# Performance work log

Hardware: AMD Instinct MI355X
Metric: run time of the kernel (lower is better)

Reference implementation:

```python
import jax, jax.numpy as jnp
import numpy as np

B, L, D = 16, 4096, 512
WORD_SIZE = 2048  # codebook_size // 4
WORD_LEN = 2


def setup_inputs() -> dict:
    key = jax.random.key(0)
    k1, k2, k3, k4, k5 = jax.random.split(key, 5)
    char_tokens = jax.random.randint(k1, (B, L), 0, 8192, dtype=jnp.int64 if jax.config.jax_enable_x64 else jnp.int32)
    char_embeddings = jax.random.normal(k2, (B, L, D), dtype=jnp.float32)
    # word_codebook initialized uniform(-1/word_size, 1/word_size) in the original
    word_codebook = jax.random.uniform(k3, (WORD_SIZE, D), dtype=jnp.float32,
                                       minval=-1.0 / WORD_SIZE, maxval=1.0 / WORD_SIZE)
    proj_w = jax.random.normal(k4, (D, D), dtype=jnp.float32) * (1.0 / np.sqrt(D))
    proj_b = jax.random.normal(k5, (D,), dtype=jnp.float32) * 0.01
    return {"char_tokens": char_tokens, "char_embeddings": char_embeddings,
            "word_codebook": word_codebook, "proj_w": proj_w, "proj_b": proj_b}


def reference(char_tokens, char_embeddings, word_codebook, proj_w, proj_b):
    Bv, Lv, Dv = char_embeddings.shape
    G = Lv // WORD_LEN  # number of 2-char groups per sequence
    # mean-pool each consecutive pair of characters -> [B, G, D]
    means = char_embeddings.reshape(Bv, G, WORD_LEN, Dv).mean(axis=2)
    # squared-euclidean nearest codebook entry (same argmin as cdist)
    # d2[b,g,k] = ||m||^2 - 2 m.W^T + ||W||^2 ; ||m||^2 constant over k -> drop
    dots = jnp.einsum('bgd,kd->bgk', means, word_codebook)            # [B,G,K]
    cb_sq = jnp.sum(word_codebook * word_codebook, axis=-1)           # [K]
    word_indices = jnp.argmin(cb_sq[None, None, :] - 2.0 * dots, axis=-1)  # [B,G]
    word_embeddings = word_codebook[word_indices]                     # [B,G,D]
    # alignment loss: mse(proj(word_emb), stop_grad(word_emb))
    projected = jnp.einsum('bgd,ed->bge', word_embeddings, proj_w) + proj_b
    target = jax.lax.stop_gradient(word_embeddings)
    alignment_loss = jnp.mean((projected - target) ** 2)
    return (word_indices, word_embeddings, alignment_loss)
```

## Files before the change

### kernel.cpp

```cpp
#include <hip/hip_runtime.h>


#define D_DIM    512
#define K_CODES  2048
#define N_ROWS   32768
#define EPS_GAP  1e-5f
#define LOSS_SCALE (1.0f / 16777216.0f)

typedef __attribute__((ext_vector_type(8))) short short8;
typedef __attribute__((ext_vector_type(4))) float f32x4;

__device__ __forceinline__ void split_bf16(float f, unsigned short& h, unsigned short& l) {
    unsigned u = __float_as_uint(f);
    h = (unsigned short)(u >> 16);
    float hr = __uint_as_float(u & 0xFFFF0000u);
    l = (unsigned short)(__float_as_uint(f - hr) >> 16);
}

__device__ __forceinline__ void dma16(const void* g, void* l) {
    __builtin_amdgcn_global_load_lds(
        (const __attribute__((address_space(1))) unsigned int*)g,
        (__attribute__((address_space(3))) unsigned int*)l, 16, 0, 0);
}

__device__ __forceinline__ void merge_cand(float s, int idx, float& v1, int& i1, float& v2, int& i2) {
    if (s < v1 || (s == v1 && idx < i1)) { v2 = v1; i2 = i1; v1 = s; i1 = idx; }
    else if (s < v2 || (s == v2 && idx < i2)) { v2 = s; i2 = idx; }
}

__global__ __launch_bounds__(256, 1)
void cra_pack_a(const float* __restrict__ ce,
                unsigned short* __restrict__ Ap)
{
    const int tid = threadIdx.x;
    const int mb  = blockIdx.x;
    const int rq  = tid >> 5;
    const int dq  = tid & 31;
    const int dbase = dq * 16;
    const int ach = dq >> 1;
    const int k0  = (dq & 1) * 16;

    #pragma unroll 2
    for (int p = 0; p < 16; ++p) {
        const int r  = p * 8 + rq;
        const int gr = mb * 128 + r;
        const float* a0 = ce + (size_t)(2 * gr) * D_DIM + dbase;
        const float* a1 = a0 + D_DIM;
        float4 x0[4], x1[4];
        #pragma unroll
        for (int q = 0; q < 4; ++q) {
            x0[q] = *(const float4*)(a0 + q * 4);
            x1[q] = *(const float4*)(a1 + q * 4);
        }
        short8 h8[2], l8[2];
        #pragma unroll
        for (int q = 0; q < 4; ++q) {
            const float m[4] = {0.5f * (x0[q].x + x1[q].x), 0.5f * (x0[q].y + x1[q].y),
                                0.5f * (x0[q].z + x1[q].z), 0.5f * (x0[q].w + x1[q].w)};
            #pragma unroll
            for (int e = 0; e < 4; ++e) {
                unsigned short hh, ll;
                split_bf16(m[e], hh, ll);
                h8[q >> 1][(q & 1) * 4 + e] = (short)hh;
                l8[q >> 1][(q & 1) * 4 + e] = (short)ll;
            }
        }
        const size_t hb = ((size_t)(mb * 32 + ach) * 128 + r) * 32 + k0;
        const size_t lb = ((size_t)(mb * 32 + 16 + ach) * 128 + r) * 32 + k0;
        *(short8*)(Ap + hb)     = h8[0];
        *(short8*)(Ap + hb + 8) = h8[1];
        *(short8*)(Ap + lb)     = l8[0];
        *(short8*)(Ap + lb + 8) = l8[1];
    }
}

__global__ __launch_bounds__(256, 1)
void cra_pack_b(const float* __restrict__ cb,
                unsigned short* __restrict__ Bp,
                float* __restrict__ cb_sq,
                float* __restrict__ Sk,
                int* __restrict__ counter,
                float* __restrict__ loss_out)
{
    __shared__ float cbs[32 * D_DIM];
    const int tid = threadIdx.x;
    const int c0  = blockIdx.x * 32;

    if (blockIdx.x == 0) {
        #pragma unroll
        for (int j = 0; j < 8; ++j) Sk[tid + j * 256] = 0.0f;
        if (tid == 0) { counter[0] = 0; loss_out[0] = 0.0f; }
    }

    {
        const float4* src = (const float4*)(cb + (size_t)c0 * D_DIM);
        float4* dst = (float4*)cbs;
        #pragma unroll
        for (int k = 0; k < 16; ++k) dst[tid + k * 256] = src[tid + k * 256];
    }
    __syncthreads();

    if (tid < 32) {
        const float* r = cbs + tid * D_DIM;
        float s = 0.f;
        for (int d = 0; d < D_DIM; ++d) s = fmaf(r[d], r[d], s);
        cb_sq[c0 + tid] = s;
    }

    const int row  = tid >> 3;
    const int k    = c0 + row;
    const int colb = k >> 7;
    const int pr   = k & 127;
    const int dspan = (tid & 7) * 64;
    #pragma unroll
    for (int g = 0; g < 8; ++g) {
        const int d   = dspan + g * 8;
        const int bch = d >> 5;
        const int k0  = d & 31;
        short8 h8, l8;
        #pragma unroll
        for (int e = 0; e < 8; ++e) {
            unsigned short hh, ll;
            split_bf16(cbs[row * D_DIM + d + e], hh, ll);
            h8[e] = (short)hh; l8[e] = (short)ll;
        }
        *(short8*)(Bp + ((size_t)(colb * 32 + bch) * 128 + pr) * 32 + k0)      = h8;
        *(short8*)(Bp + ((size_t)(colb * 32 + 16 + bch) * 128 + pr) * 32 + k0) = l8;
    }
}

__global__ __launch_bounds__(256, 1)
void cra_proj(const float* __restrict__ cb,
              const float* __restrict__ W,
              const float* __restrict__ pb,
              float* __restrict__ Sk)
{
    __shared__ float cbs[32 * D_DIM];
    __shared__ float red[4 * 32];
    const int tid = threadIdx.x;
    const int cblock = blockIdx.x >> 2;
    const int eb     = blockIdx.x & 3;
    const int c0 = cblock * 32;

    {
        const float4* src = (const float4*)(cb + (size_t)c0 * D_DIM);
        float4* dst = (float4*)cbs;
        #pragma unroll
        for (int k = 0; k < 16; ++k) dst[tid + k * 256] = src[tid + k * 256];
    }
    __syncthreads();

    const int e  = eb * 128 + (tid >> 1);
    const int dh = (tid & 1) * 256;
    float acc[32];
    #pragma unroll
    for (int c = 0; c < 32; ++c) acc[c] = 0.f;
    const float4* wrow = (const float4*)(W + (size_t)e * D_DIM + dh);
    for (int dq = 0; dq < 64; ++dq) {
        const float4 wv = wrow[dq];
        #pragma unroll
        for (int c = 0; c < 32; ++c) {
            const float4 cv = *(const float4*)&cbs[c * D_DIM + dh + dq * 4];
            acc[c] += cv.x * wv.x + cv.y * wv.y + cv.z * wv.z + cv.w * wv.w;
        }
    }
    const float bias = pb[e];
    const int w = tid >> 6;
    #pragma unroll
    for (int c = 0; c < 32; ++c) {
        const float full = acc[c] + __shfl_xor(acc[c], 1);
        const float diff = full + bias - cbs[c * D_DIM + e];
        float v = (tid & 1) ? 0.f : diff * diff;
        #pragma unroll
        for (int off = 32; off > 0; off >>= 1) v += __shfl_down(v, off, 64);
        if ((tid & 63) == 0) red[w * 32 + c] = v;
    }
    __syncthreads();
    if (tid < 32)
        atomicAdd(&Sk[c0 + tid],
                  red[tid] + red[32 + tid] + red[64 + tid] + red[96 + tid]);
}

__global__ __launch_bounds__(1024, 4)
void cra_gemm(const unsigned short* __restrict__ Ap,
              const unsigned short* __restrict__ Bp,
              const float* __restrict__ cb_sq,
              float4* __restrict__ wsRed)
{
    __shared__ __align__(16) char sMem[65536];

    const int tid  = threadIdx.x;
    const int bid  = blockIdx.x;
    const int wgid = (bid & 7) * 128 + (bid >> 3);
    const int mb   = wgid >> 3;
    const int colb = wgid & 7;
    const int rowBase = mb * 256;
    const int colBase = colb * 256;

    const int lane = tid & 63;
    const int w    = tid >> 6;
    const int wm   = w >> 2;
    const int wn   = w & 3;
    const int cid  = lane & 15;
    const int quad = lane >> 4;

    const int rg  = w >> 2;
    const int off = (w & 3) * 2048;
    const char* AgBase = (const char*)Ap + ((size_t)(2 * mb)   * 32) * 8192 + lane * 16;
    const char* BgBase = (const char*)Bp + ((size_t)(2 * colb) * 32) * 8192 + lane * 16;
    const char* gBase  = (rg < 2) ? (AgBase + (rg & 1) * (32 * 8192) + off)
                                  : (BgBase + (rg & 1) * (32 * 8192) + off);
    const int dstOff = (rg >> 1) * 16384 + (rg & 1) * 8192 + off;

    f32x4 acc[4][4];
    #pragma unroll
    for (int i = 0; i < 4; ++i)
        #pragma unroll
        for (int j = 0; j < 4; ++j) acc[i][j] = (f32x4)(0.f);

    auto stage = [&](int g, int p) {
        const int ach = g & 31;
        const int bch = (g & 15) | ((g & 32) >> 1);
        const int ch  = (rg < 2) ? ach : bch;
        const char* src = gBase + ch * 8192;
        char* dst = (char*)sMem + p * 32768 + dstOff;
        dma16(src,        dst);
        dma16(src + 1024, dst + 1024);
    };

    stage(0, 0);
    stage(1, 1);

    #pragma unroll 1
    for (int g = 0; g < 48; ++g) {
        const int p = g & 1;
        if (g < 47) asm volatile("s_waitcnt vmcnt(2)\n\ts_barrier" ::: "memory");
        else        asm volatile("s_waitcnt vmcnt(0)\n\ts_barrier" ::: "memory");

        const short* sA = (const short*)(sMem + p * 32768);
        const short* sB = (const short*)(sMem + p * 32768 + 16384);

        short8 aF[4], bF[4];
        #pragma unroll
        for (int mi = 0; mi < 4; ++mi)
            aF[mi] = *(const short8*)&sA[(wm * 64 + mi * 16 + cid) * 32 + quad * 8];
        #pragma unroll
        for (int ni = 0; ni < 4; ++ni)
            bF[ni] = *(const short8*)&sB[(wn * 64 + ni * 16 + cid) * 32 + quad * 8];
        __builtin_amdgcn_s_setprio(1);
        #pragma unroll
        for (int mi = 0; mi < 4; ++mi)
            #pragma unroll
            for (int ni = 0; ni < 4; ++ni)
                acc[mi][ni] = __builtin_amdgcn_mfma_f32_16x16x32_bf16(aF[mi], bF[ni], acc[mi][ni], 0, 0, 0);
        __builtin_amdgcn_s_setprio(0);

        asm volatile("s_waitcnt lgkmcnt(0)\n\ts_barrier" ::: "memory");

        if (g + 2 < 48) stage(g + 2, p);
    }

    float cq[4];
    #pragma unroll
    for (int ni = 0; ni < 4; ++ni) cq[ni] = cb_sq[colBase + wn * 64 + ni * 16 + cid];

    float4* sRed = (float4*)sMem;
    #pragma unroll
    for (int mi = 0; mi < 4; ++mi) {
        #pragma unroll
        for (int reg = 0; reg < 4; ++reg) {
            float v1 = 3.4e38f, v2 = 3.4e38f;
            int   i1 = 0x7FFFFFFF, i2 = 0x7FFFFFFF;
            #pragma unroll
            for (int ni = 0; ni < 4; ++ni) {
                const float s = fmaf(-2.0f, acc[mi][ni][reg], cq[ni]);
                merge_cand(s, colBase + wn * 64 + ni * 16 + cid, v1, i1, v2, i2);
            }
            #pragma unroll
            for (int d = 1; d <= 2; d <<= 1) {
                float ov1 = __shfl_xor(v1, d); int oi1 = __shfl_xor(i1, d);
                float ov2 = __shfl_xor(v2, d); int oi2 = __shfl_xor(i2, d);
                merge_cand(ov1, oi1, v1, i1, v2, i2);
                merge_cand(ov2, oi2, v1, i1, v2, i2);
            }
            if ((cid & 3) == 0) {
                const int rl = wm * 64 + mi * 16 + quad * 4 + reg;
                sRed[(rl * 4 + wn) * 4 + (cid >> 2)] =
                    make_float4(v1, __int_as_float(i1), v2, __int_as_float(i2));
            }
        }
    }
    __syncthreads();
    if (tid < 256) {
        float v1 = 3.4e38f, v2 = 3.4e38f;
        int   i1 = 0x7FFFFFFF, i2 = 0x7FFFFFFF;
        #pragma unroll
        for (int e = 0; e < 16; ++e) {
            const float4 t = sRed[tid * 16 + e];
            merge_cand(t.x, __float_as_int(t.y), v1, i1, v2, i2);
            merge_cand(t.z, __float_as_int(t.w), v1, i1, v2, i2);
        }
        wsRed[(size_t)(rowBase + tid) * 8 + colb] =
            make_float4(v1, __int_as_float(i1), v2, __int_as_float(i2));
    }
}

__global__ __launch_bounds__(256, 1)
void cra_merge(const float4* __restrict__ wsRed,
               const float* __restrict__ Sk,
               float* __restrict__ out_idx,
               float* __restrict__ out_loss,
               int* __restrict__ counter,
               int* __restrict__ flagRow,
               int2* __restrict__ flagI)
{
    __shared__ float sl[256];
    const int tid = threadIdx.x;
    const int r = blockIdx.x * 256 + tid;
    float v1 = 3.4e38f, v2 = 3.4e38f;
    int   i1 = 0x7FFFFFFF, i2 = 0x7FFFFFFF;
    #pragma unroll 4
    for (int cbk = 0; cbk < 8; ++cbk) {
        const float4 t = wsRed[(size_t)r * 8 + cbk];
        merge_cand(t.x, __float_as_int(t.y), v1, i1, v2, i2);
        merge_cand(t.z, __float_as_int(t.w), v1, i1, v2, i2);
    }
    out_idx[r] = (float)i1;
    if (v2 - v1 < EPS_GAP) {
        const int slot = atomicAdd(counter, 1);
        flagRow[slot] = r;
        flagI[slot] = make_int2(i1, i2);
    }
    sl[tid] = Sk[i1];
    __syncthreads();
    for (int s = 128; s > 0; s >>= 1) { if (tid < s) sl[tid] += sl[tid + s]; __syncthreads(); }
    if (tid == 0) atomicAdd(out_loss, sl[0] * LOSS_SCALE);
}

__global__ __launch_bounds__(256, 1)
void cra_gather(const float* __restrict__ out_idx,
                const float4* __restrict__ cb4,
                float4* __restrict__ out4)
{
    __shared__ int sidx[128];
    const int tid = threadIdx.x;
    const int rb = blockIdx.x * 128;
    if (tid < 128) sidx[tid] = (int)out_idx[rb + tid];
    __syncthreads();
    for (int j = tid; j < 128 * 128; j += 256) {
        const int row = j >> 7, q = j & 127;
        out4[(size_t)(rb + row) * 128 + q] = cb4[(size_t)sidx[row] * 128 + q];
    }
}

__global__ __launch_bounds__(256, 1)
void cra_recheck(const float* __restrict__ ce,
                 const float* __restrict__ cb,
                 const float* __restrict__ cb_sq,
                 const float* __restrict__ Sk,
                 const int* __restrict__ counter,
                 const int* __restrict__ flagRow,
                 const int2* __restrict__ flagI,
                 float* __restrict__ out_idx,
                 float4* __restrict__ out4,
                 float* __restrict__ out_loss,
                 const float4* __restrict__ cb4)
{
    __shared__ float rp[8];
    __shared__ int swin;
    const int tid = threadIdx.x;
    const int n = counter[0];
    for (int f = blockIdx.x; f < n; f += 64) {
        const int row = flagRow[f];
        const int2 ii = flagI[f];
        const int d0 = tid * 2;
        const float2 x0 = *(const float2*)(ce + (size_t)(2 * row) * D_DIM + d0);
        const float2 x1 = *(const float2*)(ce + (size_t)(2 * row) * D_DIM + D_DIM + d0);
        const float m0 = 0.5f * (x0.x + x1.x), m1 = 0.5f * (x0.y + x1.y);
        const float* c1 = cb + (size_t)ii.x * D_DIM + d0;
        const float* c2 = cb + (size_t)ii.y * D_DIM + d0;
        float p1 = fmaf(m0, c1[0], m1 * c1[1]);
        float p2 = fmaf(m0, c2[0], m1 * c2[1]);
        #pragma unroll
        for (int off = 32; off > 0; off >>= 1) {
            p1 += __shfl_down(p1, off, 64);
            p2 += __shfl_down(p2, off, 64);
        }
        if ((tid & 63) == 0) { rp[(tid >> 6) * 2] = p1; rp[(tid >> 6) * 2 + 1] = p2; }
        __syncthreads();
        if (tid == 0) {
            const float dot1 = rp[0] + rp[2] + rp[4] + rp[6];
            const float dot2 = rp[1] + rp[3] + rp[5] + rp[7];
            const float s1 = cb_sq[ii.x] - 2.f * dot1;
            const float s2 = cb_sq[ii.y] - 2.f * dot2;
            const int win = (s2 < s1 || (s2 == s1 && ii.y < ii.x)) ? ii.y : ii.x;
            swin = win;
            if (win != ii.x) {
                out_idx[row] = (float)win;
                atomicAdd(out_loss, (Sk[win] - Sk[ii.x]) * LOSS_SCALE);
            }
        }
        __syncthreads();
        if (swin != ii.x) {
            for (int q = tid; q < 128; q += 256)
                out4[(size_t)row * 128 + q] = cb4[(size_t)swin * 128 + q];
        }
        __syncthreads();
    }
}

extern "C" void kernel_launch(void* const* d_in, const int* in_sizes, int n_in,
                              void* d_out, int out_size, void* d_ws, size_t ws_size,
                              hipStream_t stream)
{
    const float* ce = (const float*)d_in[1];
    const float* cb = (const float*)d_in[2];
    const float* W  = (const float*)d_in[3];
    const float* pb = (const float*)d_in[4];

    char* ws = (char*)d_ws;
    unsigned short* Bp = (unsigned short*)ws;
    float4* wsRed  = (float4*)(ws + 4194304);
    float* cb_sq   = (float*)(ws + 12582912);
    float* Sk      = (float*)(ws + 12582912 + 8192);
    int*   flagRow = (int*)(ws + 12582912 + 16384);
    int2*  flagI   = (int2*)(ws + 12582912 + 16384 + 131072);
    int*   counter = (int*)(ws + 12582912 + 16384 + 131072 + 262144);

    float* out_idx  = (float*)d_out;
    float* out_emb  = out_idx + N_ROWS;
    float* out_loss = out_emb + (size_t)N_ROWS * D_DIM;
    unsigned short* Ap = (unsigned short*)out_emb;

    cra_pack_a<<<256, 256, 0, stream>>>(ce, Ap);
    cra_pack_b<<<64, 256, 0, stream>>>(cb, Bp, cb_sq, Sk, counter, out_loss);
    cra_proj<<<256, 256, 0, stream>>>(cb, W, pb, Sk);
    cra_gemm<<<1024, 1024, 0, stream>>>(Ap, Bp, cb_sq, wsRed);
    cra_merge<<<128, 256, 0, stream>>>(wsRed, Sk, out_idx, out_loss, counter, flagRow, flagI);
    cra_gather<<<256, 256, 0, stream>>>(out_idx, (const float4*)cb, (float4*)out_emb);
    cra_recheck<<<64, 256, 0, stream>>>(ce, cb, cb_sq, Sk, counter, flagRow, flagI,
                                        out_idx, (float4*)out_emb, out_loss, (const float4*)cb);
}
```

Measured before the change: 938.6 us.

## Shrink GEMM tile to 128x256 with triple-buffered LDS prefetch

Halves the row tile of the distance GEMM to 128 rows using 512-thread blocks and twice as many blocks. The LDS pipeline moves from double to triple buffering, with the next-but-one stage issued right after the barrier instead of at the loop end, so loads overlap more of the MFMA work. Smaller blocks may raise occupancy and help latency hiding, but they reload codebook tiles more often, raising global traffic per output.

```diff
diff --git a/kernel.cpp b/kernel.cpp
--- a/kernel.cpp
+++ b/kernel.cpp
@@ -181,21 +181,21 @@
                   red[tid] + red[32 + tid] + red[64 + tid] + red[96 + tid]);
 }
 
-__global__ __launch_bounds__(1024, 4)
+__global__ __launch_bounds__(512, 4)
 void cra_gemm(const unsigned short* __restrict__ Ap,
               const unsigned short* __restrict__ Bp,
               const float* __restrict__ cb_sq,
               float4* __restrict__ wsRed)
 {
-    __shared__ __align__(16) char sMem[65536];
+    __shared__ __align__(16) char sMem[3 * 24576];
 
     const int tid  = threadIdx.x;
     const int bid  = blockIdx.x;
-    const int wgid = (bid & 7) * 128 + (bid >> 3);
+    const int wgid = (bid & 7) * 256 + (bid >> 3);
     const int mb   = wgid >> 3;
-    const int colb = wgid & 7;
-    const int rowBase = mb * 256;
-    const int colBase = colb * 256;
+    const int cb   = wgid & 7;
+    const int rowBase = mb * 128;
+    const int colBase = cb * 256;
 
     const int lane = tid & 63;
     const int w    = tid >> 6;
@@ -204,28 +204,30 @@
     const int cid  = lane & 15;
     const int quad = lane >> 4;
 
-    const int rg  = w >> 2;
-    const int off = (w & 3) * 2048;
-    const char* AgBase = (const char*)Ap + ((size_t)(2 * mb)   * 32) * 8192 + lane * 16;
-    const char* BgBase = (const char*)Bp + ((size_t)(2 * colb) * 32) * 8192 + lane * 16;
-    const char* gBase  = (rg < 2) ? (AgBase + (rg & 1) * (32 * 8192) + off)
-                                  : (BgBase + (rg & 1) * (32 * 8192) + off);
-    const int dstOff = (rg >> 1) * 16384 + (rg & 1) * 8192 + off;
-
     f32x4 acc[4][4];
     #pragma unroll
     for (int i = 0; i < 4; ++i)
         #pragma unroll
         for (int j = 0; j < 4; ++j) acc[i][j] = (f32x4)(0.f);
+
+    const char* ApC  = (const char*)Ap + ((size_t)mb * 32) * 8192 + lane * 16;
+    const char* BpC0 = (const char*)Bp + ((size_t)(2 * cb)     * 32) * 8192 + lane * 16;
+    const char* BpC1 = (const char*)Bp + ((size_t)(2 * cb + 1) * 32) * 8192 + lane * 16;
+    const int s0 = 3 * w;
 
     auto stage = [&](int g, int p) {
         const int ach = g & 31;
         const int bch = (g & 15) | ((g & 32) >> 1);
-        const int ch  = (rg < 2) ? ach : bch;
-        const char* src = gBase + ch * 8192;
-        char* dst = (char*)sMem + p * 32768 + dstOff;
-        dma16(src,        dst);
-        dma16(src + 1024, dst + 1024);
+        char* dstBase = (char*)sMem + p * 24576;
+        #pragma unroll
+        for (int j = 0; j < 3; ++j) {
+            const int s = s0 + j;
+            const char* src;
+            if (s < 8)       src = ApC  + ach * 8192 + s * 1024;
+            else if (s < 16) src = BpC0 + bch * 8192 + (s - 8) * 1024;
+            else             src = BpC1 + bch * 8192 + (s - 16) * 1024;
+            dma16(src, dstBase + s * 1024);
+        }
     };
 
     stage(0, 0);
@@ -233,12 +235,14 @@
 
     #pragma unroll 1
     for (int g = 0; g < 48; ++g) {
-        const int p = g & 1;
-        if (g < 47) asm volatile("s_waitcnt vmcnt(2)\n\ts_barrier" ::: "memory");
+        const int p = g % 3;
+        if (g < 47) asm volatile("s_waitcnt vmcnt(3)\n\ts_barrier" ::: "memory");
         else        asm volatile("s_waitcnt vmcnt(0)\n\ts_barrier" ::: "memory");
 
-        const short* sA = (const short*)(sMem + p * 32768);
-        const short* sB = (const short*)(sMem + p * 32768 + 16384);
+        if (g + 2 < 48) stage(g + 2, (g + 2) % 3);
+
+        const short* sA = (const short*)(sMem + p * 24576);
+        const short* sB = (const short*)(sMem + p * 24576 + 8192 + (wn >> 1) * 8192);
 
         short8 aF[4], bF[4];
         #pragma unroll
@@ -246,7 +250,7 @@
             aF[mi] = *(const short8*)&sA[(wm * 64 + mi * 16 + cid) * 32 + quad * 8];
         #pragma unroll
         for (int ni = 0; ni < 4; ++ni)
-            bF[ni] = *(const short8*)&sB[(wn * 64 + ni * 16 + cid) * 32 + quad * 8];
+            bF[ni] = *(const short8*)&sB[((wn & 1) * 64 + ni * 16 + cid) * 32 + quad * 8];
         __builtin_amdgcn_s_setprio(1);
         #pragma unroll
         for (int mi = 0; mi < 4; ++mi)
@@ -256,14 +260,13 @@
         __builtin_amdgcn_s_setprio(0);
 
         asm volatile("s_waitcnt lgkmcnt(0)\n\ts_barrier" ::: "memory");
-
-        if (g + 2 < 48) stage(g + 2, p);
     }
 
     float cq[4];
     #pragma unroll
     for (int ni = 0; ni < 4; ++ni) cq[ni] = cb_sq[colBase + wn * 64 + ni * 16 + cid];
 
+    __syncthreads();
     float4* sRed = (float4*)sMem;
     #pragma unroll
     for (int mi = 0; mi < 4; ++mi) {
@@ -284,14 +287,14 @@
                 merge_cand(ov2, oi2, v1, i1, v2, i2);
             }
             if ((cid & 3) == 0) {
-                const int rl = wm * 64 + mi * 16 + quad * 4 + reg;
-                sRed[(rl * 4 + wn) * 4 + (cid >> 2)] =
+                const int row = wm * 64 + mi * 16 + quad * 4 + reg;
+                sRed[(row * 4 + wn) * 4 + (cid >> 2)] =
                     make_float4(v1, __int_as_float(i1), v2, __int_as_float(i2));
             }
         }
     }
     __syncthreads();
-    if (tid < 256) {
+    if (tid < 128) {
         float v1 = 3.4e38f, v2 = 3.4e38f;
         int   i1 = 0x7FFFFFFF, i2 = 0x7FFFFFFF;
         #pragma unroll
@@ -300,7 +303,7 @@
             merge_cand(t.x, __float_as_int(t.y), v1, i1, v2, i2);
             merge_cand(t.z, __float_as_int(t.w), v1, i1, v2, i2);
         }
-        wsRed[(size_t)(rowBase + tid) * 8 + colb] =
+        wsRed[(size_t)(rowBase + tid) * 8 + cb] =
             make_float4(v1, __int_as_float(i1), v2, __int_as_float(i2));
     }
 }
@@ -435,7 +438,7 @@
     cra_pack_a<<<256, 256, 0, stream>>>(ce, Ap);
     cra_pack_b<<<64, 256, 0, stream>>>(cb, Bp, cb_sq, Sk, counter, out_loss);
     cra_proj<<<256, 256, 0, stream>>>(cb, W, pb, Sk);
-    cra_gemm<<<1024, 1024, 0, stream>>>(Ap, Bp, cb_sq, wsRed);
+    cra_gemm<<<2048, 512, 0, stream>>>(Ap, Bp, cb_sq, wsRed);
     cra_merge<<<128, 256, 0, stream>>>(wsRed, Sk, out_idx, out_loss, counter, flagRow, flagI);
     cra_gather<<<256, 256, 0, stream>>>(out_idx, (const float4*)cb, (float4*)out_emb);
     cra_recheck<<<64, 256, 0, stream>>>(ce, cb, cb_sq, Sk, counter, flagRow, flagI,
```

After: 872.7 us. -7.0%, faster.
